# Performance work log

Measured on AMD Instinct MI355X. Metric: run time of the kernel, lower is better.

The kernel has to match this reference:

```python
import jax, jax.numpy as jnp
import numpy as np

B, L, HID = 16, 512, 768
HEADS, M = 12, 4
EMB, BLK, NER, NCLS = 768, 8, 6, 97


def setup_inputs() -> dict:
    key = jax.random.key(0)
    ks = jax.random.split(key, 10)
    return {
        "sequence_output": jax.random.normal(ks[0], (B, L, HID), jnp.float32),
        "attention": jax.random.uniform(ks[1], (B, HEADS, L, L), jnp.float32),
        "entity_pos": jax.random.randint(ks[2], (B, 2, M), 0, L - 2),
        "hs_ner_tags": jax.random.uniform(ks[3], (B, NER), jnp.float32),
        "ts_ner_tags": jax.random.uniform(ks[4], (B, NER), jnp.float32),
        "Wh": jax.random.normal(ks[5], (EMB, 2 * HID + NER), jnp.float32) * 0.02,
        "bh": jnp.zeros((EMB,), jnp.float32),
        "Wt": jax.random.normal(ks[6], (EMB, 2 * HID + NER), jnp.float32) * 0.02,
        "bt": jnp.zeros((EMB,), jnp.float32),
        "Wb": jax.random.normal(ks[7], (NCLS, EMB * BLK), jnp.float32) * 0.02,
        "bb": jnp.zeros((NCLS,), jnp.float32),
    }


def reference(sequence_output, attention, entity_pos, hs_ner_tags, ts_ner_tags,
              Wh, bh, Wt, bt, Wb, bb):
    b_idx = jnp.arange(B)[:, None, None]            # [B,1,1]
    starts = entity_pos + 1                         # [B,2,M] (all < L by construction)

    # entity embeddings: gather mention token embeddings, logsumexp-pool over mentions
    ment_emb = sequence_output[b_idx, starts]       # [B,2,M,HID]
    ent_emb = jax.scipy.special.logsumexp(ment_emb, axis=2)  # [B,2,HID]

    # entity attentions: gather mention attention rows, mean-pool over mentions
    attn_t = attention.transpose(0, 2, 1, 3)        # [B,L,HEADS,L]
    ment_att = attn_t[b_idx, starts]                # [B,2,M,HEADS,L]
    ent_att = ment_att.mean(axis=2)                 # [B,2,HEADS,L]

    hs, ts = ent_emb[:, 0], ent_emb[:, 1]           # [B,HID]
    h_att, t_att = ent_att[:, 0], ent_att[:, 1]     # [B,HEADS,L]

    ht_att = (h_att * t_att).mean(axis=1)           # [B,L]
    ht_att = ht_att / (ht_att.sum(axis=1, keepdims=True) + 1e-5)
    rs = jnp.einsum('bld,bl->bd', sequence_output, ht_att)  # [B,HID]

    hs2 = jnp.tanh(jnp.concatenate([hs, rs, hs_ner_tags], axis=1) @ Wh.T + bh)
    ts2 = jnp.tanh(jnp.concatenate([ts, rs, ts_ner_tags], axis=1) @ Wt.T + bt)

    b1 = hs2.reshape(B, EMB // BLK, BLK)
    b2 = ts2.reshape(B, EMB // BLK, BLK)
    bl = (b1[:, :, :, None] * b2[:, :, None, :]).reshape(B, EMB * BLK)
    logits = bl @ Wb.T + bb                         # [B, NCLS]
    return logits
```

## Files before the change

### kernel.cpp

```cpp
#include <hip/hip_runtime.h>
#include <math.h>

#define B 16
#define L 512
#define HID 768
#define HEADS 12
#define M 4
#define EMB 768
#define BLK 8
#define NER 6
#define NCLS 97
#define CAT (2*HID + NER)
#define EB (EMB*BLK)
#define NCH 8

__global__ void k_att(const float* __restrict__ att, const float* __restrict__ seq,
                      const int* __restrict__ epos,
                      float* __restrict__ pp, float* __restrict__ ent,
                      float* __restrict__ rs) {
    int b = blockIdx.x, h = blockIdx.y;
    __shared__ int ss[2][M];
    if (threadIdx.x < 2*M) {
        int e = threadIdx.x >> 2, m = threadIdx.x & 3;
        ss[e][m] = epos[(b*2+e)*M + m] + 1;
    }
    __syncthreads();

    int l = threadIdx.x;
    const float* ah = att + ((size_t)b*HEADS + h)*L*L;
    float a0 = 0.f, a1 = 0.f;
    #pragma unroll
    for (int m = 0; m < M; ++m) {
        a0 += ah[(size_t)ss[0][m]*L + l];
        a1 += ah[(size_t)ss[1][m]*L + l];
    }
    pp[((size_t)b*HEADS + h)*L + l] = a0*a1;

    if (h < 2) {
        const float* base = seq + (size_t)b*L*HID;
        for (int d = threadIdx.x; d < HID; d += 512) {
            float v0 = base[(size_t)ss[h][0]*HID + d];
            float v1 = base[(size_t)ss[h][1]*HID + d];
            float v2 = base[(size_t)ss[h][2]*HID + d];
            float v3 = base[(size_t)ss[h][3]*HID + d];
            float mx = fmaxf(fmaxf(v0, v1), fmaxf(v2, v3));
            float s = expf(v0-mx) + expf(v1-mx) + expf(v2-mx) + expf(v3-mx);
            ent[((size_t)h*B + b)*HID + d] = mx + logf(s);
        }
    } else if (h == 2) {
        for (int d = threadIdx.x; d < HID; d += 512) rs[b*HID + d] = 0.f;
    }
}

__launch_bounds__(192)
__global__ void k_rs(const float* __restrict__ seq, const float* __restrict__ pp,
                     float* __restrict__ rs) {
    int b = blockIdx.x, ch = blockIdx.y;
    __shared__ float sraw[L];
    __shared__ float red[3];
    __shared__ float sinv;
    float psum = 0.f;
    for (int l = threadIdx.x; l < L; l += 192) {
        float r = 0.f;
        #pragma unroll
        for (int h = 0; h < HEADS; ++h) r += pp[((size_t)b*HEADS + h)*L + l];
        r *= (1.f/(M*M*HEADS));
        sraw[l] = r;
        psum += r;
    }
    for (int off = 32; off; off >>= 1) psum += __shfl_down(psum, off);
    int wid = threadIdx.x >> 6, lane = threadIdx.x & 63;
    if (lane == 0) red[wid] = psum;
    __syncthreads();
    if (threadIdx.x == 0) sinv = 1.f/(red[0] + red[1] + red[2] + 1e-5f);
    __syncthreads();
    float inv = sinv;

    const float4* sp = (const float4*)(seq + (size_t)b*L*HID + (size_t)ch*(L/NCH)*HID);
    float4 acc = make_float4(0.f, 0.f, 0.f, 0.f);
    for (int i = 0; i < L/NCH; ++i) {
        float w = sraw[ch*(L/NCH) + i] * inv;
        float4 v = sp[i*(HID/4) + threadIdx.x];
        acc.x += v.x*w; acc.y += v.y*w; acc.z += v.z*w; acc.w += v.w*w;
    }
    float* rp = rs + b*HID + threadIdx.x*4;
    atomicAdd(rp+0, acc.x);
    atomicAdd(rp+1, acc.y);
    atomicAdd(rp+2, acc.z);
    atomicAdd(rp+3, acc.w);
}

__launch_bounds__(512)
__global__ void k_proj(const float* __restrict__ Wh, const float* __restrict__ bh,
                       const float* __restrict__ Wt, const float* __restrict__ bt,
                       const float* __restrict__ ent, const float* __restrict__ rs,
                       const float* __restrict__ hner, const float* __restrict__ tner,
                       float* __restrict__ out) {
    int t = blockIdx.y, zh = blockIdx.z;
    __shared__ float actA[CAT*4];
    __shared__ float actB[CAT*4];
    const float* e0  = ent + (size_t)t*B*HID;
    const float* ner = t ? tner : hner;
    for (int idx = threadIdx.x; idx < CAT*8; idx += 512) {
        int k = idx >> 3, bi = idx & 7;
        int gb = zh*8 + bi;
        float v;
        if (k < HID)            v = e0[gb*HID + k];
        else if (k < 2*HID)     v = rs[gb*HID + (k - HID)];
        else                    v = ner[gb*NER + (k - 2*HID)];
        if (bi < 4) actA[k*4 + bi] = v; else actB[k*4 + bi - 4] = v;
    }
    __syncthreads();

    int wid = threadIdx.x >> 6, lane = threadIdx.x & 63;
    int j = blockIdx.x*8 + wid;
    const float* wrow = (t ? Wt : Wh) + (size_t)j*CAT;
    float acc[8];
    #pragma unroll
    for (int b = 0; b < 8; ++b) acc[b] = 0.f;
    for (int i = 0; i < 25; ++i) {
        int k = i*64 + lane;
        if (k < CAT) {
            float w = wrow[k];
            float4 a = *(const float4*)&actA[k*4];
            float4 c = *(const float4*)&actB[k*4];
            acc[0] += w*a.x; acc[1] += w*a.y; acc[2] += w*a.z; acc[3] += w*a.w;
            acc[4] += w*c.x; acc[5] += w*c.y; acc[6] += w*c.z; acc[7] += w*c.w;
        }
    }
    for (int off = 32; off; off >>= 1)
        #pragma unroll
        for (int b = 0; b < 8; ++b) acc[b] += __shfl_down(acc[b], off);
    if (lane == 0) {
        float bj = (t ? bt : bh)[j];
        #pragma unroll
        for (int b = 0; b < 8; ++b)
            out[((size_t)t*B + zh*8 + b)*EMB + j] = tanhf(acc[b] + bj);
    }
}

__global__ void k_bl(const float* __restrict__ proj, float* __restrict__ bl) {
    int b = blockIdx.x;
    const float* ph = proj + (size_t)b*EMB;
    const float* pt = proj + (size_t)B*EMB + (size_t)b*EMB;
    for (int i4 = threadIdx.x; i4 < EB/4; i4 += 512) {
        int k = i4*4;
        int g = k >> 6, r = (k >> 3) & 7, c0 = k & 7;
        float pr = ph[g*8 + r];
        float4 q = *(const float4*)(pt + g*8 + c0);
        float4 o = make_float4(pr*q.x, pr*q.y, pr*q.z, pr*q.w);
        ((float4*)(bl + (size_t)b*EB))[i4] = o;
    }
}

__launch_bounds__(512)
__global__ void k_logits(const float* __restrict__ Wb, const float* __restrict__ bb,
                         const float* __restrict__ bl, float* __restrict__ out) {
    int c = blockIdx.x;
    const float4* wr = (const float4*)(Wb + (size_t)c*EB);
    float acc[B];
    #pragma unroll
    for (int b = 0; b < B; ++b) acc[b] = 0.f;
    for (int i = threadIdx.x; i < EB/4; i += 512) {
        float4 w = wr[i];
        #pragma unroll
        for (int b = 0; b < B; ++b) {
            float4 v = ((const float4*)(bl + (size_t)b*EB))[i];
            acc[b] += w.x*v.x + w.y*v.y + w.z*v.z + w.w*v.w;
        }
    }
    int wid = threadIdx.x >> 6, lane = threadIdx.x & 63;
    for (int off = 32; off; off >>= 1)
        #pragma unroll
        for (int b = 0; b < B; ++b) acc[b] += __shfl_down(acc[b], off);
    __shared__ float partl[8][B];
    if (lane == 0)
        #pragma unroll
        for (int b = 0; b < B; ++b) partl[wid][b] = acc[b];
    __syncthreads();
    if (threadIdx.x < B) {
        int b = threadIdx.x;
        float s = 0.f;
        #pragma unroll
        for (int w = 0; w < 8; ++w) s += partl[w][b];
        out[b*NCLS + c] = s + bb[c];
    }
}

extern "C" void kernel_launch(void* const* d_in, const int* in_sizes, int n_in,
                              void* d_out, int out_size, void* d_ws, size_t ws_size,
                              hipStream_t stream) {
    const float* seq  = (const float*)d_in[0];
    const float* att  = (const float*)d_in[1];
    const int*   epos = (const int*)  d_in[2];
    const float* hner = (const float*)d_in[3];
    const float* tner = (const float*)d_in[4];
    const float* Wh   = (const float*)d_in[5];
    const float* bh   = (const float*)d_in[6];
    const float* Wt   = (const float*)d_in[7];
    const float* bt   = (const float*)d_in[8];
    const float* Wb   = (const float*)d_in[9];
    const float* bb   = (const float*)d_in[10];
    float* out = (float*)d_out;

    float* ws   = (float*)d_ws;
    float* pp   = ws;
    float* ent  = pp   + (size_t)B*HEADS*L;
    float* rs   = ent  + 2*B*HID;
    float* proj = rs   + B*HID;
    float* bl   = proj + 2*B*EMB;

    k_att   <<<dim3(B, HEADS), 512, 0, stream>>>(att, seq, epos, pp, ent, rs);
    k_rs    <<<dim3(B, NCH),   192, 0, stream>>>(seq, pp, rs);
    k_proj  <<<dim3(EMB/8, 2, 2), 512, 0, stream>>>(Wh, bh, Wt, bt, ent, rs, hner, tner, proj);
    k_bl    <<<dim3(B),        512, 0, stream>>>(proj, bl);
    k_logits<<<dim3(NCLS),     512, 0, stream>>>(Wb, bb, bl, out);
}
```

Before: 298.5 us.

## Fuse all stages into one cooperative persistent kernel with grid syncs

Replaces five kernel launches with a single cooperative kernel of 256 blocks that runs each stage and separates them with grid-wide syncs. It also folds the bilinear outer-product materialization into the logits loop, computing products on the fly instead of writing and rereading the bl buffer. The projection stage now has each wave compute two output rows, and the rs reduction is split into 16 chunks. The aim is to remove launch gaps and intermediate traffic, at the cost of grid-sync overhead, less parallelism in later stages, and extra shared-memory use that limits occupancy.

Result: slower. 542.8 us (+81.8%).

```diff
diff --git a/kernel.cpp b/kernel.cpp
--- a/kernel.cpp
+++ b/kernel.cpp
@@ -1,5 +1,8 @@
 #include <hip/hip_runtime.h>
+#include <hip/hip_cooperative_groups.h>
 #include <math.h>
+
+namespace cg = cooperative_groups;
 
 #define B 16
 #define L 512
@@ -12,178 +15,208 @@
 #define NCLS 97
 #define CAT (2*HID + NER)
 #define EB (EMB*BLK)
-#define NCH 8
-
-__global__ void k_att(const float* __restrict__ att, const float* __restrict__ seq,
-                      const int* __restrict__ epos,
-                      float* __restrict__ pp, float* __restrict__ ent,
-                      float* __restrict__ rs) {
-    int b = blockIdx.x, h = blockIdx.y;
-    __shared__ int ss[2][M];
-    if (threadIdx.x < 2*M) {
-        int e = threadIdx.x >> 2, m = threadIdx.x & 3;
-        ss[e][m] = epos[(b*2+e)*M + m] + 1;
-    }
-    __syncthreads();
-
-    int l = threadIdx.x;
-    const float* ah = att + ((size_t)b*HEADS + h)*L*L;
-    float a0 = 0.f, a1 = 0.f;
-    #pragma unroll
-    for (int m = 0; m < M; ++m) {
-        a0 += ah[(size_t)ss[0][m]*L + l];
-        a1 += ah[(size_t)ss[1][m]*L + l];
-    }
-    pp[((size_t)b*HEADS + h)*L + l] = a0*a1;
-
-    if (h < 2) {
-        const float* base = seq + (size_t)b*L*HID;
-        for (int d = threadIdx.x; d < HID; d += 512) {
-            float v0 = base[(size_t)ss[h][0]*HID + d];
-            float v1 = base[(size_t)ss[h][1]*HID + d];
-            float v2 = base[(size_t)ss[h][2]*HID + d];
-            float v3 = base[(size_t)ss[h][3]*HID + d];
-            float mx = fmaxf(fmaxf(v0, v1), fmaxf(v2, v3));
-            float s = expf(v0-mx) + expf(v1-mx) + expf(v2-mx) + expf(v3-mx);
-            ent[((size_t)h*B + b)*HID + d] = mx + logf(s);
-        }
-    } else if (h == 2) {
-        for (int d = threadIdx.x; d < HID; d += 512) rs[b*HID + d] = 0.f;
-    }
-}
-
-__launch_bounds__(192)
-__global__ void k_rs(const float* __restrict__ seq, const float* __restrict__ pp,
-                     float* __restrict__ rs) {
-    int b = blockIdx.x, ch = blockIdx.y;
+#define NB 256
+#define NT 512
+#define NCH 16
+#define LCH (L/NCH)
+
+__launch_bounds__(NT)
+__global__ void mega(const float* __restrict__ att, const float* __restrict__ seq,
+                     const int* __restrict__ epos,
+                     const float* __restrict__ hner, const float* __restrict__ tner,
+                     const float* __restrict__ Wh, const float* __restrict__ bh,
+                     const float* __restrict__ Wt, const float* __restrict__ bt,
+                     const float* __restrict__ Wb, const float* __restrict__ bb,
+                     float* __restrict__ pp, float* __restrict__ ent,
+                     float* __restrict__ rs, float* __restrict__ proj,
+                     float* __restrict__ out) {
+    cg::grid_group gg = cg::this_grid();
+    const int blk = blockIdx.x, tid = threadIdx.x;
+
+    __shared__ int   ss[2][M];
     __shared__ float sraw[L];
-    __shared__ float red[3];
+    __shared__ float red[8];
     __shared__ float sinv;
-    float psum = 0.f;
-    for (int l = threadIdx.x; l < L; l += 192) {
+    __shared__ float actA[CAT*4];
+    __shared__ float actB[CAT*4];
+
+    if (blk < B*HEADS) {
+        int b = blk / HEADS, h = blk - b*HEADS;
+        if (tid < 2*M) {
+            int e = tid >> 2, m = tid & 3;
+            ss[e][m] = epos[(b*2 + e)*M + m] + 1;
+        }
+        __syncthreads();
+
+        int l = tid;
+        const float* ah = att + ((size_t)b*HEADS + h)*L*L;
+        float a0 = 0.f, a1 = 0.f;
+        #pragma unroll
+        for (int m = 0; m < M; ++m) {
+            a0 += ah[(size_t)ss[0][m]*L + l];
+            a1 += ah[(size_t)ss[1][m]*L + l];
+        }
+        pp[((size_t)b*HEADS + h)*L + l] = a0*a1;
+
+        if (h < 2) {
+            const float* base = seq + (size_t)b*L*HID;
+            for (int d = tid; d < HID; d += NT) {
+                float v0 = base[(size_t)ss[h][0]*HID + d];
+                float v1 = base[(size_t)ss[h][1]*HID + d];
+                float v2 = base[(size_t)ss[h][2]*HID + d];
+                float v3 = base[(size_t)ss[h][3]*HID + d];
+                float mx = fmaxf(fmaxf(v0, v1), fmaxf(v2, v3));
+                float s = expf(v0-mx) + expf(v1-mx) + expf(v2-mx) + expf(v3-mx);
+                ent[((size_t)h*B + b)*HID + d] = mx + logf(s);
+            }
+        }
+    } else if (blk < B*HEADS + B) {
+        int b = blk - B*HEADS;
+        for (int d = tid; d < HID; d += NT) rs[b*HID + d] = 0.f;
+    }
+    __threadfence();
+    gg.sync();
+
+    {
+        int b = blk >> 4, ch = blk & (NCH-1);
+        int l = tid;
         float r = 0.f;
         #pragma unroll
         for (int h = 0; h < HEADS; ++h) r += pp[((size_t)b*HEADS + h)*L + l];
         r *= (1.f/(M*M*HEADS));
         sraw[l] = r;
-        psum += r;
-    }
-    for (int off = 32; off; off >>= 1) psum += __shfl_down(psum, off);
-    int wid = threadIdx.x >> 6, lane = threadIdx.x & 63;
-    if (lane == 0) red[wid] = psum;
-    __syncthreads();
-    if (threadIdx.x == 0) sinv = 1.f/(red[0] + red[1] + red[2] + 1e-5f);
-    __syncthreads();
-    float inv = sinv;
-
-    const float4* sp = (const float4*)(seq + (size_t)b*L*HID + (size_t)ch*(L/NCH)*HID);
-    float4 acc = make_float4(0.f, 0.f, 0.f, 0.f);
-    for (int i = 0; i < L/NCH; ++i) {
-        float w = sraw[ch*(L/NCH) + i] * inv;
-        float4 v = sp[i*(HID/4) + threadIdx.x];
-        acc.x += v.x*w; acc.y += v.y*w; acc.z += v.z*w; acc.w += v.w*w;
-    }
-    float* rp = rs + b*HID + threadIdx.x*4;
-    atomicAdd(rp+0, acc.x);
-    atomicAdd(rp+1, acc.y);
-    atomicAdd(rp+2, acc.z);
-    atomicAdd(rp+3, acc.w);
-}
-
-__launch_bounds__(512)
-__global__ void k_proj(const float* __restrict__ Wh, const float* __restrict__ bh,
-                       const float* __restrict__ Wt, const float* __restrict__ bt,
-                       const float* __restrict__ ent, const float* __restrict__ rs,
-                       const float* __restrict__ hner, const float* __restrict__ tner,
-                       float* __restrict__ out) {
-    int t = blockIdx.y, zh = blockIdx.z;
-    __shared__ float actA[CAT*4];
-    __shared__ float actB[CAT*4];
-    const float* e0  = ent + (size_t)t*B*HID;
-    const float* ner = t ? tner : hner;
-    for (int idx = threadIdx.x; idx < CAT*8; idx += 512) {
-        int k = idx >> 3, bi = idx & 7;
-        int gb = zh*8 + bi;
-        float v;
-        if (k < HID)            v = e0[gb*HID + k];
-        else if (k < 2*HID)     v = rs[gb*HID + (k - HID)];
-        else                    v = ner[gb*NER + (k - 2*HID)];
-        if (bi < 4) actA[k*4 + bi] = v; else actB[k*4 + bi - 4] = v;
-    }
-    __syncthreads();
-
-    int wid = threadIdx.x >> 6, lane = threadIdx.x & 63;
-    int j = blockIdx.x*8 + wid;
-    const float* wrow = (t ? Wt : Wh) + (size_t)j*CAT;
-    float acc[8];
-    #pragma unroll
-    for (int b = 0; b < 8; ++b) acc[b] = 0.f;
-    for (int i = 0; i < 25; ++i) {
-        int k = i*64 + lane;
-        if (k < CAT) {
-            float w = wrow[k];
-            float4 a = *(const float4*)&actA[k*4];
-            float4 c = *(const float4*)&actB[k*4];
-            acc[0] += w*a.x; acc[1] += w*a.y; acc[2] += w*a.z; acc[3] += w*a.w;
-            acc[4] += w*c.x; acc[5] += w*c.y; acc[6] += w*c.z; acc[7] += w*c.w;
-        }
-    }
-    for (int off = 32; off; off >>= 1)
-        #pragma unroll
-        for (int b = 0; b < 8; ++b) acc[b] += __shfl_down(acc[b], off);
-    if (lane == 0) {
-        float bj = (t ? bt : bh)[j];
-        #pragma unroll
-        for (int b = 0; b < 8; ++b)
-            out[((size_t)t*B + zh*8 + b)*EMB + j] = tanhf(acc[b] + bj);
-    }
-}
-
-__global__ void k_bl(const float* __restrict__ proj, float* __restrict__ bl) {
-    int b = blockIdx.x;
-    const float* ph = proj + (size_t)b*EMB;
-    const float* pt = proj + (size_t)B*EMB + (size_t)b*EMB;
-    for (int i4 = threadIdx.x; i4 < EB/4; i4 += 512) {
-        int k = i4*4;
-        int g = k >> 6, r = (k >> 3) & 7, c0 = k & 7;
-        float pr = ph[g*8 + r];
-        float4 q = *(const float4*)(pt + g*8 + c0);
-        float4 o = make_float4(pr*q.x, pr*q.y, pr*q.z, pr*q.w);
-        ((float4*)(bl + (size_t)b*EB))[i4] = o;
-    }
-}
-
-__launch_bounds__(512)
-__global__ void k_logits(const float* __restrict__ Wb, const float* __restrict__ bb,
-                         const float* __restrict__ bl, float* __restrict__ out) {
-    int c = blockIdx.x;
-    const float4* wr = (const float4*)(Wb + (size_t)c*EB);
-    float acc[B];
-    #pragma unroll
-    for (int b = 0; b < B; ++b) acc[b] = 0.f;
-    for (int i = threadIdx.x; i < EB/4; i += 512) {
-        float4 w = wr[i];
-        #pragma unroll
-        for (int b = 0; b < B; ++b) {
-            float4 v = ((const float4*)(bl + (size_t)b*EB))[i];
-            acc[b] += w.x*v.x + w.y*v.y + w.z*v.z + w.w*v.w;
-        }
-    }
-    int wid = threadIdx.x >> 6, lane = threadIdx.x & 63;
-    for (int off = 32; off; off >>= 1)
-        #pragma unroll
-        for (int b = 0; b < B; ++b) acc[b] += __shfl_down(acc[b], off);
-    __shared__ float partl[8][B];
-    if (lane == 0)
-        #pragma unroll
-        for (int b = 0; b < B; ++b) partl[wid][b] = acc[b];
-    __syncthreads();
-    if (threadIdx.x < B) {
-        int b = threadIdx.x;
-        float s = 0.f;
-        #pragma unroll
-        for (int w = 0; w < 8; ++w) s += partl[w][b];
-        out[b*NCLS + c] = s + bb[c];
+
+        float psum = r;
+        for (int off = 32; off; off >>= 1) psum += __shfl_down(psum, off);
+        int wid = tid >> 6, lane = tid & 63;
+        if (lane == 0) red[wid] = psum;
+        __syncthreads();
+        if (tid == 0) {
+            float s = 0.f;
+            #pragma unroll
+            for (int w = 0; w < 8; ++w) s += red[w];
+            sinv = 1.f/(s + 1e-5f);
+        }
+        __syncthreads();
+        float inv = sinv;
+
+        if (tid < 384) {
+            int lsub = tid / 192, d4 = tid - lsub*192;
+            const float4* sp = (const float4*)(seq + (size_t)b*L*HID);
+            int l0 = ch*LCH + lsub*(LCH/2);
+            float4 acc = make_float4(0.f, 0.f, 0.f, 0.f);
+            #pragma unroll
+            for (int i = 0; i < LCH/2; ++i) {
+                int ll = l0 + i;
+                float w = sraw[ll]*inv;
+                float4 v = sp[(size_t)ll*(HID/4) + d4];
+                acc.x += w*v.x; acc.y += w*v.y; acc.z += w*v.z; acc.w += w*v.w;
+            }
+            float* rp = rs + b*HID + d4*4;
+            atomicAdd(rp+0, acc.x);
+            atomicAdd(rp+1, acc.y);
+            atomicAdd(rp+2, acc.z);
+            atomicAdd(rp+3, acc.w);
+        }
+    }
+    __threadfence();
+    gg.sync();
+
+    if (blk < 192) {
+        int jg = blk >> 2, t = (blk >> 1) & 1, zh = blk & 1;
+        const float* e0  = ent + (size_t)t*B*HID;
+        const float* ner = t ? tner : hner;
+        for (int idx = tid; idx < CAT*8; idx += NT) {
+            int k = idx >> 3, bi = idx & 7;
+            int gb = zh*8 + bi;
+            float v;
+            if (k < HID)            v = e0[gb*HID + k];
+            else if (k < 2*HID)     v = rs[gb*HID + (k - HID)];
+            else                    v = ner[gb*NER + (k - 2*HID)];
+            if (bi < 4) actA[k*4 + bi] = v; else actB[k*4 + (bi-4)] = v;
+        }
+        __syncthreads();
+
+        int wid = tid >> 6, lane = tid & 63;
+        int j0 = jg*16 + wid*2;
+        const float* wbase = (t ? Wt : Wh);
+        const float* w0 = wbase + (size_t)j0*CAT;
+        const float* w1 = w0 + CAT;
+        float acc0[8], acc1[8];
+        #pragma unroll
+        for (int b = 0; b < 8; ++b) { acc0[b] = 0.f; acc1[b] = 0.f; }
+        for (int i = 0; i < 25; ++i) {
+            int k = i*64 + lane;
+            if (k < CAT) {
+                float wa = w0[k], wb = w1[k];
+                float4 a = *(const float4*)&actA[k*4];
+                float4 c = *(const float4*)&actB[k*4];
+                acc0[0] += wa*a.x; acc0[1] += wa*a.y; acc0[2] += wa*a.z; acc0[3] += wa*a.w;
+                acc0[4] += wa*c.x; acc0[5] += wa*c.y; acc0[6] += wa*c.z; acc0[7] += wa*c.w;
+                acc1[0] += wb*a.x; acc1[1] += wb*a.y; acc1[2] += wb*a.z; acc1[3] += wb*a.w;
+                acc1[4] += wb*c.x; acc1[5] += wb*c.y; acc1[6] += wb*c.z; acc1[7] += wb*c.w;
+            }
+        }
+        for (int off = 32; off; off >>= 1) {
+            #pragma unroll
+            for (int b = 0; b < 8; ++b) {
+                acc0[b] += __shfl_down(acc0[b], off);
+                acc1[b] += __shfl_down(acc1[b], off);
+            }
+        }
+        if (lane == 0) {
+            float bj0 = (t ? bt : bh)[j0];
+            float bj1 = (t ? bt : bh)[j0+1];
+            #pragma unroll
+            for (int b = 0; b < 8; ++b) {
+                size_t row = ((size_t)t*B + zh*8 + b)*EMB;
+                proj[row + j0]     = tanhf(acc0[b] + bj0);
+                proj[row + j0 + 1] = tanhf(acc1[b] + bj1);
+            }
+        }
+    }
+    __threadfence();
+    gg.sync();
+
+    if (blk < NCLS) {
+        int c = blk;
+        const float4* wr = (const float4*)(Wb + (size_t)c*EB);
+        const float* ph = proj;
+        const float* pt = proj + (size_t)B*EMB;
+        float acc[B];
+        #pragma unroll
+        for (int b = 0; b < B; ++b) acc[b] = 0.f;
+        for (int i = tid; i < EB/4; i += NT) {
+            float4 w = wr[i];
+            int k  = i*4;
+            int g8 = (k >> 6)*8;
+            int r  = (k >> 3) & 7;
+            int c0 = k & 7;
+            #pragma unroll
+            for (int b = 0; b < B; ++b) {
+                float pr = ph[b*EMB + g8 + r];
+                float4 q = *(const float4*)(pt + b*EMB + g8 + c0);
+                acc[b] += pr*(w.x*q.x + w.y*q.y + w.z*q.z + w.w*q.w);
+            }
+        }
+        int wid = tid >> 6, lane = tid & 63;
+        for (int off = 32; off; off >>= 1) {
+            #pragma unroll
+            for (int b = 0; b < B; ++b) acc[b] += __shfl_down(acc[b], off);
+        }
+        __shared__ float partl[8][B];
+        if (lane == 0) {
+            #pragma unroll
+            for (int b = 0; b < B; ++b) partl[wid][b] = acc[b];
+        }
+        __syncthreads();
+        if (tid < B) {
+            int b = tid;
+            float s = 0.f;
+            #pragma unroll
+            for (int w = 0; w < 8; ++w) s += partl[w][b];
+            out[b*NCLS + c] = s + bb[c];
+        }
     }
 }
 
@@ -208,11 +241,13 @@
     float* ent  = pp   + (size_t)B*HEADS*L;
     float* rs   = ent  + 2*B*HID;
     float* proj = rs   + B*HID;
-    float* bl   = proj + 2*B*EMB;
-
-    k_att   <<<dim3(B, HEADS), 512, 0, stream>>>(att, seq, epos, pp, ent, rs);
-    k_rs    <<<dim3(B, NCH),   192, 0, stream>>>(seq, pp, rs);
-    k_proj  <<<dim3(EMB/8, 2, 2), 512, 0, stream>>>(Wh, bh, Wt, bt, ent, rs, hner, tner, proj);
-    k_bl    <<<dim3(B),        512, 0, stream>>>(proj, bl);
-    k_logits<<<dim3(NCLS),     512, 0, stream>>>(Wb, bb, bl, out);
+
+    void* kargs[] = {
+        (void*)&att, (void*)&seq, (void*)&epos,
+        (void*)&hner, (void*)&tner,
+        (void*)&Wh, (void*)&bh, (void*)&Wt, (void*)&bt,
+        (void*)&Wb, (void*)&bb,
+        (void*)&pp, (void*)&ent, (void*)&rs, (void*)&proj, (void*)&out
+    };
+    hipLaunchCooperativeKernel((void*)mega, dim3(NB), dim3(NT), kargs, 0, stream);
 }
```

## Fuse bilinear outer product into logits kernel and double rs chunking

Applied to the files above, without the earlier changes.

Removes the separate bilinear kernel and its intermediate buffer by computing head*tail products on the fly inside the logits reduction from the projection outputs. This drops one launch and the global write/read of the expanded bilinear tensor, at the cost of redundant multiplies and less regular loads per class block. Also doubles the number of sequence chunks in the rs reduction to spread work over more blocks, adding more atomics.

After: 300.9 us. About the same (+0.8%).

```diff
diff --git a/kernel.cpp b/kernel.cpp
--- a/kernel.cpp
+++ b/kernel.cpp
@@ -12,7 +12,8 @@
 #define NCLS 97
 #define CAT (2*HID + NER)
 #define EB (EMB*BLK)
-#define NCH 8
+#define NCH 16
+#define LCH (L/NCH)
 
 __global__ void k_att(const float* __restrict__ att, const float* __restrict__ seq,
                       const int* __restrict__ epos,
@@ -76,10 +77,10 @@
     __syncthreads();
     float inv = sinv;
 
-    const float4* sp = (const float4*)(seq + (size_t)b*L*HID + (size_t)ch*(L/NCH)*HID);
+    const float4* sp = (const float4*)(seq + (size_t)b*L*HID + (size_t)ch*LCH*HID);
     float4 acc = make_float4(0.f, 0.f, 0.f, 0.f);
-    for (int i = 0; i < L/NCH; ++i) {
-        float w = sraw[ch*(L/NCH) + i] * inv;
+    for (int i = 0; i < LCH; ++i) {
+        float w = sraw[ch*LCH + i] * inv;
         float4 v = sp[i*(HID/4) + threadIdx.x];
         acc.x += v.x*w; acc.y += v.y*w; acc.z += v.z*w; acc.w += v.w*w;
     }
@@ -139,34 +140,27 @@
     }
 }
 
-__global__ void k_bl(const float* __restrict__ proj, float* __restrict__ bl) {
-    int b = blockIdx.x;
-    const float* ph = proj + (size_t)b*EMB;
-    const float* pt = proj + (size_t)B*EMB + (size_t)b*EMB;
-    for (int i4 = threadIdx.x; i4 < EB/4; i4 += 512) {
-        int k = i4*4;
-        int g = k >> 6, r = (k >> 3) & 7, c0 = k & 7;
-        float pr = ph[g*8 + r];
-        float4 q = *(const float4*)(pt + g*8 + c0);
-        float4 o = make_float4(pr*q.x, pr*q.y, pr*q.z, pr*q.w);
-        ((float4*)(bl + (size_t)b*EB))[i4] = o;
-    }
-}
-
 __launch_bounds__(512)
 __global__ void k_logits(const float* __restrict__ Wb, const float* __restrict__ bb,
-                         const float* __restrict__ bl, float* __restrict__ out) {
+                         const float* __restrict__ proj, float* __restrict__ out) {
     int c = blockIdx.x;
     const float4* wr = (const float4*)(Wb + (size_t)c*EB);
+    const float* ph = proj;
+    const float* pt = proj + (size_t)B*EMB;
     float acc[B];
     #pragma unroll
     for (int b = 0; b < B; ++b) acc[b] = 0.f;
     for (int i = threadIdx.x; i < EB/4; i += 512) {
         float4 w = wr[i];
+        int k  = i*4;
+        int g8 = (k >> 6)*8;
+        int r  = (k >> 3) & 7;
+        int c0 = k & 7;
         #pragma unroll
         for (int b = 0; b < B; ++b) {
-            float4 v = ((const float4*)(bl + (size_t)b*EB))[i];
-            acc[b] += w.x*v.x + w.y*v.y + w.z*v.z + w.w*v.w;
+            float pr = ph[b*EMB + g8 + r];
+            float4 q = *(const float4*)(pt + b*EMB + g8 + c0);
+            acc[b] += pr*(w.x*q.x + w.y*q.y + w.z*q.z + w.w*q.w);
         }
     }
     int wid = threadIdx.x >> 6, lane = threadIdx.x & 63;
@@ -208,11 +202,9 @@
     float* ent  = pp   + (size_t)B*HEADS*L;
     float* rs   = ent  + 2*B*HID;
     float* proj = rs   + B*HID;
-    float* bl   = proj + 2*B*EMB;
 
     k_att   <<<dim3(B, HEADS), 512, 0, stream>>>(att, seq, epos, pp, ent, rs);
     k_rs    <<<dim3(B, NCH),   192, 0, stream>>>(seq, pp, rs);
     k_proj  <<<dim3(EMB/8, 2, 2), 512, 0, stream>>>(Wh, bh, Wt, bt, ent, rs, hner, tner, proj);
-    k_bl    <<<dim3(B),        512, 0, stream>>>(proj, bl);
-    k_logits<<<dim3(NCLS),     512, 0, stream>>>(Wb, bb, bl, out);
-}
+    k_logits<<<dim3(NCLS),     512, 0, stream>>>(Wb, bb, proj, out);
+}
```
